# Kernel optimization log

Measured on AMD Instinct MI355X. Metric: run time of the kernel, lower is better.

The kernel has to match this reference:

```python
import jax, jax.numpy as jnp
import numpy as np


def setup_inputs() -> dict:
    key = jax.random.key(0)
    k1, k2 = jax.random.split(key)
    x = jax.random.normal(k1, (64, 64, 64, 64), dtype=jnp.float32)
    embeddings = jax.random.normal(k2, (400, 64), dtype=jnp.float32) * 0.1
    return {"x": x, "embeddings": embeddings}


def reference(x, embeddings):
    D = embeddings.shape[1]
    flat_x = x.reshape(-1, D)  # [N, D]
    # squared L2 distance via sum-of-squares + matmul: [N, K]
    distances = (
        jnp.sum(flat_x * flat_x, axis=1, keepdims=True)
        + jnp.sum(embeddings * embeddings, axis=1)
        - 2.0 * jnp.matmul(flat_x, embeddings.T)
    )
    encoding_indices = jnp.argmin(distances, axis=1)  # [N]
    quantized = jnp.take(embeddings, encoding_indices, axis=0)  # [N, D]
    return quantized.reshape(x.shape)
```

## Files before the change

### kernel.cpp

```cpp
#include <hip/hip_runtime.h>
#include <hip/hip_bf16.h>

#define D 64
#define K 400
#define KT 25
#define BLOCK 1024
#define WPB (BLOCK / 64)

typedef _Float16 f16x8 __attribute__((ext_vector_type(8)));
typedef float f32x4 __attribute__((ext_vector_type(4)));

__global__ __launch_bounds__(BLOCK, 4) void vq_mfma(
    const float* __restrict__ x,
    const float* __restrict__ emb,
    float* __restrict__ out,
    int nrows) {
  __shared__ __align__(16) _Float16 sB[KT][4][64][8];
  __shared__ float s_norm[K];

  const int tid = threadIdx.x;

  for (int e = tid; e < KT * 4 * 64; e += BLOCK) {
    int t = e >> 8;
    int f = (e >> 6) & 3;
    int l = e & 63;
    int code = t * 16 + (l & 15);
    int kb = ((l >> 4) << 3) + ((f >> 1) << 5);
    const float* ep = emb + code * D + kb;
    float v[8];
    *(float4*)&v[0] = *(const float4*)ep;
    *(float4*)&v[4] = *(const float4*)(ep + 4);
    _Float16 h[8];
    if ((f & 1) == 0) {
#pragma unroll
      for (int j = 0; j < 8; ++j) h[j] = (_Float16)(2.0f * v[j]);
    } else {
#pragma unroll
      for (int j = 0; j < 8; ++j) {
        float s = 2.0f * v[j];
        _Float16 hh = (_Float16)s;
        float r = s - (float)hh;
        h[j] = (_Float16)(r * 2048.0f);
      }
    }
    *(f16x8*)&sB[t][f][l][0] = *(f16x8*)&h[0];
  }
  for (int k = tid; k < K; k += BLOCK) {
    const float* ep = emb + k * D;
    float s = 0.f;
#pragma unroll
    for (int d = 0; d < D; ++d) s = fmaf(ep[d], ep[d], s);
    s_norm[k] = s;
  }
  __syncthreads();

  const int lane = tid & 63;
  const int wid = tid >> 6;
  const int gw = blockIdx.x * WPB + wid;
  const int nw = gridDim.x * WPB;
  const int l15 = lane & 15;
  const int q = lane >> 4;

  const int npair = nrows >> 5;
  for (int p = gw; p < npair; p += nw) {
    const int row0 = p << 5;

    f16x8 xh[2][2], xl[2][2];
#pragma unroll
    for (int a = 0; a < 2; ++a)
#pragma unroll
      for (int c = 0; c < 2; ++c) {
        const float* xp =
            x + (size_t)(row0 + a * 16 + l15) * D + q * 8 + c * 32;
        float v[8];
        *(float4*)&v[0] = *(const float4*)xp;
        *(float4*)&v[4] = *(const float4*)(xp + 4);
        _Float16 hh[8], ll[8];
#pragma unroll
        for (int j = 0; j < 8; ++j) {
          _Float16 h = (_Float16)v[j];
          float r = v[j] - (float)h;
          hh[j] = h;
          ll[j] = (_Float16)(r * 2048.0f);
        }
        xh[a][c] = *(f16x8*)&hh[0];
        xl[a][c] = *(f16x8*)&ll[0];
      }

    float bestm[2][4];
    int bestt[2][4];
#pragma unroll
    for (int a = 0; a < 2; ++a)
#pragma unroll
      for (int i = 0; i < 4; ++i) {
        bestm[a][i] = -3.4e38f;
        bestt[a][i] = 0;
      }

    for (int t = 0; t < KT; ++t) {
      f16x8 bh0 = *(const f16x8*)&sB[t][0][lane][0];
      f16x8 bl0 = *(const f16x8*)&sB[t][1][lane][0];
      f16x8 bh1 = *(const f16x8*)&sB[t][2][lane][0];
      f16x8 bl1 = *(const f16x8*)&sB[t][3][lane][0];
      float nrm = s_norm[t * 16 + l15];
#pragma unroll
      for (int a = 0; a < 2; ++a) {
        f32x4 ah = {0.f, 0.f, 0.f, 0.f};
        f32x4 al = {0.f, 0.f, 0.f, 0.f};
        ah = __builtin_amdgcn_mfma_f32_16x16x32_f16(xh[a][0], bh0, ah, 0, 0, 0);
        ah = __builtin_amdgcn_mfma_f32_16x16x32_f16(xh[a][1], bh1, ah, 0, 0, 0);
        al = __builtin_amdgcn_mfma_f32_16x16x32_f16(xh[a][0], bl0, al, 0, 0, 0);
        al = __builtin_amdgcn_mfma_f32_16x16x32_f16(xl[a][0], bh0, al, 0, 0, 0);
        al = __builtin_amdgcn_mfma_f32_16x16x32_f16(xh[a][1], bl1, al, 0, 0, 0);
        al = __builtin_amdgcn_mfma_f32_16x16x32_f16(xl[a][1], bh1, al, 0, 0, 0);
#pragma unroll
        for (int i = 0; i < 4; ++i) {
          float dv = fmaf(al[i], 4.8828125e-4f, ah[i]);
          float m = dv - nrm;
          bool gt = m > bestm[a][i];
          bestm[a][i] = gt ? m : bestm[a][i];
          bestt[a][i] = gt ? t : bestt[a][i];
        }
      }
    }

#pragma unroll
    for (int a = 0; a < 2; ++a) {
      float bv[4];
      int bk[4];
#pragma unroll
      for (int i = 0; i < 4; ++i) {
        bv[i] = bestm[a][i];
        bk[i] = bestt[a][i] * 16 + l15;
      }
#pragma unroll
      for (int m = 1; m <= 8; m <<= 1) {
#pragma unroll
        for (int i = 0; i < 4; ++i) {
          float ov = __shfl_xor(bv[i], m, 64);
          int ok = __shfl_xor(bk[i], m, 64);
          bool take = (ov > bv[i]) || ((ov == bv[i]) && (ok < bk[i]));
          bv[i] = take ? ov : bv[i];
          bk[i] = take ? ok : bk[i];
        }
      }
      int j = (lane >> 2) & 3;
      int k01 = (j & 1) ? bk[1] : bk[0];
      int k23 = (j & 1) ? bk[3] : bk[2];
      int kk = (j & 2) ? k23 : k01;
      int r = row0 + a * 16 + (lane >> 2);
      const float4* src = (const float4*)(emb + kk * D + (lane & 3) * 16);
      float4* dst = (float4*)(out + (size_t)r * D + (lane & 3) * 16);
#pragma unroll
      for (int s = 0; s < 4; ++s) dst[s] = src[s];
    }
  }
}

extern "C" void kernel_launch(void* const* d_in, const int* in_sizes, int n_in,
                              void* d_out, int out_size, void* d_ws, size_t ws_size,
                              hipStream_t stream) {
  const float* x = (const float*)d_in[0];
  const float* emb = (const float*)d_in[1];
  float* out = (float*)d_out;
  int nrows = in_sizes[0] / D;
  vq_mfma<<<256, BLOCK, 0, stream>>>(x, emb, out, nrows);
}
```

Baseline: 148.5 us.

## Double-buffer codebook LDS loads, fold norm into MFMA accumulator, nontemporal interleaved stores

Software-pipelines the codebook tile loop so the LDS fragments for the next tile are loaded while the MFMAs for the current tile run. The negated code norm now seeds the high accumulator, which removes a subtract per element. The output copy uses interleaved float4 indices across lanes with nontemporal stores to improve coalescing and avoid cache pollution. The norm precompute is vectorized with float4 loads. The extra live fragments raise register pressure under the 1024-thread launch bound.

```diff
diff --git a/kernel.cpp b/kernel.cpp
--- a/kernel.cpp
+++ b/kernel.cpp
@@ -1,5 +1,4 @@
 #include <hip/hip_runtime.h>
-#include <hip/hip_bf16.h>
 
 #define D 64
 #define K 400
@@ -46,11 +45,17 @@
     *(f16x8*)&sB[t][f][l][0] = *(f16x8*)&h[0];
   }
   for (int k = tid; k < K; k += BLOCK) {
-    const float* ep = emb + k * D;
-    float s = 0.f;
+    const float4* ep = (const float4*)(emb + (size_t)k * D);
+    float4 s4 = {0.f, 0.f, 0.f, 0.f};
 #pragma unroll
-    for (int d = 0; d < D; ++d) s = fmaf(ep[d], ep[d], s);
-    s_norm[k] = s;
+    for (int d = 0; d < 16; ++d) {
+      float4 v = ep[d];
+      s4.x = fmaf(v.x, v.x, s4.x);
+      s4.y = fmaf(v.y, v.y, s4.y);
+      s4.z = fmaf(v.z, v.z, s4.z);
+      s4.w = fmaf(v.w, v.w, s4.w);
+    }
+    s_norm[k] = (s4.x + s4.y) + (s4.z + s4.w);
   }
   __syncthreads();
 
@@ -60,6 +65,36 @@
   const int nw = gridDim.x * WPB;
   const int l15 = lane & 15;
   const int q = lane >> 4;
+
+#define LOADB(Bf, Nf, T)                           \
+  do {                                             \
+    Bf##0 = *(const f16x8*)&sB[(T)][0][lane][0];   \
+    Bf##1 = *(const f16x8*)&sB[(T)][1][lane][0];   \
+    Bf##2 = *(const f16x8*)&sB[(T)][2][lane][0];   \
+    Bf##3 = *(const f16x8*)&sB[(T)][3][lane][0];   \
+    Nf = s_norm[(T) * 16 + l15];                   \
+  } while (0)
+
+#define PROC(Bf, Nf, T)                                                        \
+  do {                                                                         \
+    const float nn_ = -(Nf);                                                   \
+    _Pragma("unroll") for (int a_ = 0; a_ < 2; ++a_) {                         \
+      f32x4 ah = {nn_, nn_, nn_, nn_};                                         \
+      f32x4 al = {0.f, 0.f, 0.f, 0.f};                                         \
+      ah = __builtin_amdgcn_mfma_f32_16x16x32_f16(xh[a_][0], Bf##0, ah, 0, 0, 0); \
+      ah = __builtin_amdgcn_mfma_f32_16x16x32_f16(xh[a_][1], Bf##2, ah, 0, 0, 0); \
+      al = __builtin_amdgcn_mfma_f32_16x16x32_f16(xh[a_][0], Bf##1, al, 0, 0, 0); \
+      al = __builtin_amdgcn_mfma_f32_16x16x32_f16(xl[a_][0], Bf##0, al, 0, 0, 0); \
+      al = __builtin_amdgcn_mfma_f32_16x16x32_f16(xh[a_][1], Bf##3, al, 0, 0, 0); \
+      al = __builtin_amdgcn_mfma_f32_16x16x32_f16(xl[a_][1], Bf##2, al, 0, 0, 0); \
+      _Pragma("unroll") for (int i_ = 0; i_ < 4; ++i_) {                       \
+        float m_ = fmaf(al[i_], 4.8828125e-4f, ah[i_]);  \
+        bool gt_ = m_ > bestm[a_][i_];                                         \
+        bestm[a_][i_] = gt_ ? m_ : bestm[a_][i_];                              \
+        bestt[a_][i_] = gt_ ? (T) : bestt[a_][i_];                             \
+      }                                                                        \
+    }                                                                          \
+  } while (0)
 
   const int npair = nrows >> 5;
   for (int p = gw; p < npair; p += nw) {
@@ -97,32 +132,16 @@
         bestt[a][i] = 0;
       }
 
-    for (int t = 0; t < KT; ++t) {
-      f16x8 bh0 = *(const f16x8*)&sB[t][0][lane][0];
-      f16x8 bl0 = *(const f16x8*)&sB[t][1][lane][0];
-      f16x8 bh1 = *(const f16x8*)&sB[t][2][lane][0];
-      f16x8 bl1 = *(const f16x8*)&sB[t][3][lane][0];
-      float nrm = s_norm[t * 16 + l15];
-#pragma unroll
-      for (int a = 0; a < 2; ++a) {
-        f32x4 ah = {0.f, 0.f, 0.f, 0.f};
-        f32x4 al = {0.f, 0.f, 0.f, 0.f};
-        ah = __builtin_amdgcn_mfma_f32_16x16x32_f16(xh[a][0], bh0, ah, 0, 0, 0);
-        ah = __builtin_amdgcn_mfma_f32_16x16x32_f16(xh[a][1], bh1, ah, 0, 0, 0);
-        al = __builtin_amdgcn_mfma_f32_16x16x32_f16(xh[a][0], bl0, al, 0, 0, 0);
-        al = __builtin_amdgcn_mfma_f32_16x16x32_f16(xl[a][0], bh0, al, 0, 0, 0);
-        al = __builtin_amdgcn_mfma_f32_16x16x32_f16(xh[a][1], bl1, al, 0, 0, 0);
-        al = __builtin_amdgcn_mfma_f32_16x16x32_f16(xl[a][1], bh1, al, 0, 0, 0);
-#pragma unroll
-        for (int i = 0; i < 4; ++i) {
-          float dv = fmaf(al[i], 4.8828125e-4f, ah[i]);
-          float m = dv - nrm;
-          bool gt = m > bestm[a][i];
-          bestm[a][i] = gt ? m : bestm[a][i];
-          bestt[a][i] = gt ? t : bestt[a][i];
-        }
-      }
+    f16x8 bA0, bA1, bA2, bA3, bB0, bB1, bB2, bB3;
+    float nA, nB;
+    LOADB(bA, nA, 0);
+    for (int t2 = 0; t2 < 12; ++t2) {
+      LOADB(bB, nB, 2 * t2 + 1);
+      PROC(bA, nA, 2 * t2);
+      LOADB(bA, nA, 2 * t2 + 2);
+      PROC(bB, nB, 2 * t2 + 1);
     }
+    PROC(bA, nA, 24);
 
 #pragma unroll
     for (int a = 0; a < 2; ++a) {
@@ -149,12 +168,18 @@
       int k23 = (j & 1) ? bk[3] : bk[2];
       int kk = (j & 2) ? k23 : k01;
       int r = row0 + a * 16 + (lane >> 2);
-      const float4* src = (const float4*)(emb + kk * D + (lane & 3) * 16);
-      float4* dst = (float4*)(out + (size_t)r * D + (lane & 3) * 16);
+      const f32x4* src = (const f32x4*)(emb + (size_t)kk * D);
+      f32x4* dst = (f32x4*)(out + (size_t)r * D);
 #pragma unroll
-      for (int s = 0; s < 4; ++s) dst[s] = src[s];
+      for (int s = 0; s < 4; ++s) {
+        int idx = (lane & 3) + (s << 2);
+        f32x4 v = src[idx];
+        __builtin_nontemporal_store(v, &dst[idx]);
+      }
     }
   }
+#undef LOADB
+#undef PROC
 }
 
 extern "C" void kernel_launch(void* const* d_in, const int* in_sizes, int n_in,
```

Measured after the change: 148.5 us. No clear change (+0.0%).

## Process 64 rows per wave and fold code norms into MFMA accumulator init

Applied to the files above, without the earlier changes.

Each wave now handles four 16-row tiles instead of two, so every LDS load of codebook fragments feeds twice as many MFMAs. The negated code norm is used as the initial accumulator value, which removes a subtraction per element. The shuffle reductions are interleaved across tiles, and output copies are reordered so the four lanes of a row write adjacent float4s, which coalesces the stores. The cost is more live registers under a 1024-thread launch bound, and with 262144 rows split into 4096 groups over 4096 waves each wave now runs a single iteration.

```diff
diff --git a/kernel.cpp b/kernel.cpp
--- a/kernel.cpp
+++ b/kernel.cpp
@@ -1,5 +1,4 @@
 #include <hip/hip_runtime.h>
-#include <hip/hip_bf16.h>
 
 #define D 64
 #define K 400
@@ -9,6 +8,15 @@
 
 typedef _Float16 f16x8 __attribute__((ext_vector_type(8)));
 typedef float f32x4 __attribute__((ext_vector_type(4)));
+
+
+#define SPL(hh, ll, j, val)                          \
+  do {                                               \
+    float v_ = (val);                                \
+    _Float16 t_ = (_Float16)v_;                      \
+    (hh)[j] = t_;                                    \
+    (ll)[j] = (_Float16)((v_ - (float)t_) * 2048.0f);\
+  } while (0)
 
 __global__ __launch_bounds__(BLOCK, 4) void vq_mfma(
     const float* __restrict__ x,
@@ -27,30 +35,43 @@
     int code = t * 16 + (l & 15);
     int kb = ((l >> 4) << 3) + ((f >> 1) << 5);
     const float* ep = emb + code * D + kb;
-    float v[8];
-    *(float4*)&v[0] = *(const float4*)ep;
-    *(float4*)&v[4] = *(const float4*)(ep + 4);
-    _Float16 h[8];
+    float4 u = *(const float4*)ep;
+    float4 w = *(const float4*)(ep + 4);
+    f16x8 h;
     if ((f & 1) == 0) {
-#pragma unroll
-      for (int j = 0; j < 8; ++j) h[j] = (_Float16)(2.0f * v[j]);
+      h[0] = (_Float16)(2.0f * u.x);
+      h[1] = (_Float16)(2.0f * u.y);
+      h[2] = (_Float16)(2.0f * u.z);
+      h[3] = (_Float16)(2.0f * u.w);
+      h[4] = (_Float16)(2.0f * w.x);
+      h[5] = (_Float16)(2.0f * w.y);
+      h[6] = (_Float16)(2.0f * w.z);
+      h[7] = (_Float16)(2.0f * w.w);
     } else {
-#pragma unroll
-      for (int j = 0; j < 8; ++j) {
-        float s = 2.0f * v[j];
-        _Float16 hh = (_Float16)s;
-        float r = s - (float)hh;
-        h[j] = (_Float16)(r * 2048.0f);
-      }
+#define LOC(j, val)                                    \
+      do {                                             \
+        float s_ = 2.0f * (val);                       \
+        _Float16 t_ = (_Float16)s_;                    \
+        h[j] = (_Float16)((s_ - (float)t_) * 2048.0f); \
+      } while (0)
+      LOC(0, u.x); LOC(1, u.y); LOC(2, u.z); LOC(3, u.w);
+      LOC(4, w.x); LOC(5, w.y); LOC(6, w.z); LOC(7, w.w);
+#undef LOC
     }
-    *(f16x8*)&sB[t][f][l][0] = *(f16x8*)&h[0];
+    *(f16x8*)&sB[t][f][l][0] = h;
   }
   for (int k = tid; k < K; k += BLOCK) {
-    const float* ep = emb + k * D;
-    float s = 0.f;
+    const float4* ep = (const float4*)(emb + (size_t)k * D);
+    float4 s4 = {0.f, 0.f, 0.f, 0.f};
 #pragma unroll
-    for (int d = 0; d < D; ++d) s = fmaf(ep[d], ep[d], s);
-    s_norm[k] = s;
+    for (int d = 0; d < 16; ++d) {
+      float4 v = ep[d];
+      s4.x = fmaf(v.x, v.x, s4.x);
+      s4.y = fmaf(v.y, v.y, s4.y);
+      s4.z = fmaf(v.z, v.z, s4.z);
+      s4.w = fmaf(v.w, v.w, s4.w);
+    }
+    s_norm[k] = (s4.x + s4.y) + (s4.z + s4.w);
   }
   __syncthreads();
 
@@ -61,36 +82,36 @@
   const int l15 = lane & 15;
   const int q = lane >> 4;
 
-  const int npair = nrows >> 5;
-  for (int p = gw; p < npair; p += nw) {
-    const int row0 = p << 5;
+  const int ngrp = nrows >> 6;
+  for (int g = gw; g < ngrp; g += nw) {
+    const int row0 = g << 6;
 
-    f16x8 xh[2][2], xl[2][2];
+    f16x8 xh[4][2], xl[4][2];
 #pragma unroll
-    for (int a = 0; a < 2; ++a)
+    for (int a = 0; a < 4; ++a)
 #pragma unroll
       for (int c = 0; c < 2; ++c) {
         const float* xp =
             x + (size_t)(row0 + a * 16 + l15) * D + q * 8 + c * 32;
-        float v[8];
-        *(float4*)&v[0] = *(const float4*)xp;
-        *(float4*)&v[4] = *(const float4*)(xp + 4);
-        _Float16 hh[8], ll[8];
-#pragma unroll
-        for (int j = 0; j < 8; ++j) {
-          _Float16 h = (_Float16)v[j];
-          float r = v[j] - (float)h;
-          hh[j] = h;
-          ll[j] = (_Float16)(r * 2048.0f);
-        }
-        xh[a][c] = *(f16x8*)&hh[0];
-        xl[a][c] = *(f16x8*)&ll[0];
+        float4 u = *(const float4*)xp;
+        float4 w = *(const float4*)(xp + 4);
+        f16x8 hh, ll;
+        SPL(hh, ll, 0, u.x);
+        SPL(hh, ll, 1, u.y);
+        SPL(hh, ll, 2, u.z);
+        SPL(hh, ll, 3, u.w);
+        SPL(hh, ll, 4, w.x);
+        SPL(hh, ll, 5, w.y);
+        SPL(hh, ll, 6, w.z);
+        SPL(hh, ll, 7, w.w);
+        xh[a][c] = hh;
+        xl[a][c] = ll;
       }
 
-    float bestm[2][4];
-    int bestt[2][4];
+    float bestm[4][4];
+    int bestt[4][4];
 #pragma unroll
-    for (int a = 0; a < 2; ++a)
+    for (int a = 0; a < 4; ++a)
 #pragma unroll
       for (int i = 0; i < 4; ++i) {
         bestm[a][i] = -3.4e38f;
@@ -98,25 +119,24 @@
       }
 
     for (int t = 0; t < KT; ++t) {
-      f16x8 bh0 = *(const f16x8*)&sB[t][0][lane][0];
-      f16x8 bl0 = *(const f16x8*)&sB[t][1][lane][0];
-      f16x8 bh1 = *(const f16x8*)&sB[t][2][lane][0];
-      f16x8 bl1 = *(const f16x8*)&sB[t][3][lane][0];
-      float nrm = s_norm[t * 16 + l15];
+      f16x8 b0 = *(const f16x8*)&sB[t][0][lane][0];
+      f16x8 b1 = *(const f16x8*)&sB[t][1][lane][0];
+      f16x8 b2 = *(const f16x8*)&sB[t][2][lane][0];
+      f16x8 b3 = *(const f16x8*)&sB[t][3][lane][0];
+      float nn = -s_norm[t * 16 + l15];
 #pragma unroll
-      for (int a = 0; a < 2; ++a) {
-        f32x4 ah = {0.f, 0.f, 0.f, 0.f};
+      for (int a = 0; a < 4; ++a) {
+        f32x4 ah = {nn, nn, nn, nn};
         f32x4 al = {0.f, 0.f, 0.f, 0.f};
-        ah = __builtin_amdgcn_mfma_f32_16x16x32_f16(xh[a][0], bh0, ah, 0, 0, 0);
-        ah = __builtin_amdgcn_mfma_f32_16x16x32_f16(xh[a][1], bh1, ah, 0, 0, 0);
-        al = __builtin_amdgcn_mfma_f32_16x16x32_f16(xh[a][0], bl0, al, 0, 0, 0);
-        al = __builtin_amdgcn_mfma_f32_16x16x32_f16(xl[a][0], bh0, al, 0, 0, 0);
-        al = __builtin_amdgcn_mfma_f32_16x16x32_f16(xh[a][1], bl1, al, 0, 0, 0);
-        al = __builtin_amdgcn_mfma_f32_16x16x32_f16(xl[a][1], bh1, al, 0, 0, 0);
+        ah = __builtin_amdgcn_mfma_f32_16x16x32_f16(xh[a][0], b0, ah, 0, 0, 0);
+        ah = __builtin_amdgcn_mfma_f32_16x16x32_f16(xh[a][1], b2, ah, 0, 0, 0);
+        al = __builtin_amdgcn_mfma_f32_16x16x32_f16(xh[a][0], b1, al, 0, 0, 0);
+        al = __builtin_amdgcn_mfma_f32_16x16x32_f16(xl[a][0], b0, al, 0, 0, 0);
+        al = __builtin_amdgcn_mfma_f32_16x16x32_f16(xh[a][1], b3, al, 0, 0, 0);
+        al = __builtin_amdgcn_mfma_f32_16x16x32_f16(xl[a][1], b2, al, 0, 0, 0);
 #pragma unroll
         for (int i = 0; i < 4; ++i) {
-          float dv = fmaf(al[i], 4.8828125e-4f, ah[i]);
-          float m = dv - nrm;
+          float m = fmaf(al[i], 4.8828125e-4f, ah[i]);
           bool gt = m > bestm[a][i];
           bestm[a][i] = gt ? m : bestm[a][i];
           bestt[a][i] = gt ? t : bestt[a][i];
@@ -124,35 +144,42 @@
       }
     }
 
+    float bv[4][4];
+    int bk[4][4];
 #pragma unroll
-    for (int a = 0; a < 2; ++a) {
-      float bv[4];
-      int bk[4];
+    for (int a = 0; a < 4; ++a)
 #pragma unroll
       for (int i = 0; i < 4; ++i) {
-        bv[i] = bestm[a][i];
-        bk[i] = bestt[a][i] * 16 + l15;
+        bv[a][i] = bestm[a][i];
+        bk[a][i] = bestt[a][i] * 16 + l15;
       }
 #pragma unroll
-      for (int m = 1; m <= 8; m <<= 1) {
+    for (int m = 1; m <= 8; m <<= 1) {
+#pragma unroll
+      for (int a = 0; a < 4; ++a)
 #pragma unroll
         for (int i = 0; i < 4; ++i) {
-          float ov = __shfl_xor(bv[i], m, 64);
-          int ok = __shfl_xor(bk[i], m, 64);
-          bool take = (ov > bv[i]) || ((ov == bv[i]) && (ok < bk[i]));
-          bv[i] = take ? ov : bv[i];
-          bk[i] = take ? ok : bk[i];
+          float ov = __shfl_xor(bv[a][i], m, 64);
+          int ok = __shfl_xor(bk[a][i], m, 64);
+          bool take = (ov > bv[a][i]) || ((ov == bv[a][i]) && (ok < bk[a][i]));
+          bv[a][i] = take ? ov : bv[a][i];
+          bk[a][i] = take ? ok : bk[a][i];
         }
-      }
+    }
+#pragma unroll
+    for (int a = 0; a < 4; ++a) {
       int j = (lane >> 2) & 3;
-      int k01 = (j & 1) ? bk[1] : bk[0];
-      int k23 = (j & 1) ? bk[3] : bk[2];
+      int k01 = (j & 1) ? bk[a][1] : bk[a][0];
+      int k23 = (j & 1) ? bk[a][3] : bk[a][2];
       int kk = (j & 2) ? k23 : k01;
       int r = row0 + a * 16 + (lane >> 2);
-      const float4* src = (const float4*)(emb + kk * D + (lane & 3) * 16);
-      float4* dst = (float4*)(out + (size_t)r * D + (lane & 3) * 16);
+      const f32x4* src = (const f32x4*)(emb + (size_t)kk * D);
+      f32x4* dst = (f32x4*)(out + (size_t)r * D);
 #pragma unroll
-      for (int s = 0; s < 4; ++s) dst[s] = src[s];
+      for (int s = 0; s < 4; ++s) {
+        int idx = (lane & 3) + (s << 2);
+        dst[idx] = src[idx];
+      }
     }
   }
 }
```

New measurement: 175.3 us. 18.1% more time.
